# Kernel optimization log

Measured on AMD Instinct MI355X. Metric: run time of the kernel, lower is better.

The kernel has to match this reference:

```python
import jax, jax.numpy as jnp
import numpy as np

HEADS = 4
DIM_HEAD = 32


def setup_inputs() -> dict:
    key = jax.random.key(0)
    k1, k2, k3, k4 = jax.random.split(key, 4)
    b, dim, t = 8, 64, 16384
    inner = HEADS * DIM_HEAD  # 128
    x = jax.random.normal(k1, (b, dim, t), dtype=jnp.float32)
    # Conv1d(dim, inner*3, kernel=1, bias=False) -> weight (3*inner, dim)
    w_qkv = jax.random.normal(k2, (3 * inner, dim), dtype=jnp.float32) * (1.0 / np.sqrt(dim))
    # Conv1d(inner, dim, kernel=1) -> weight (dim, inner), bias (dim,)
    w_out = jax.random.normal(k3, (dim, inner), dtype=jnp.float32) * (1.0 / np.sqrt(inner))
    b_out = jax.random.normal(k4, (dim,), dtype=jnp.float32) * 0.01
    return {"x": x, "w_qkv": w_qkv, "w_out": w_out, "b_out": b_out}


def reference(x, w_qkv, w_out, b_out):
    b, c, t = x.shape
    h, dh = HEADS, DIM_HEAD
    # 1x1 conv == per-timestep matmul: (b, 3*inner, t)
    qkv = jnp.einsum('oc,bct->bot', w_qkv, x)
    q, k, v = jnp.split(qkv, 3, axis=1)
    q = q.reshape(b, h, dh, t)
    k = k.reshape(b, h, dh, t)
    v = v.reshape(b, h, dh, t)
    q = jax.nn.softmax(q, axis=-1)   # softmax over time
    k = jax.nn.softmax(k, axis=-2)   # softmax over head-dim d
    # einsum('bhdt,bhds->bhds', k, v): sums k over t, broadcast-scales v
    context = jnp.einsum('bhdt,bhds->bhds', k, v)
    # einsum('bhdt,bhds->bhdt', q, context): sums context over s, scales q
    out = jnp.einsum('bhdt,bhds->bhdt', q, context)
    out = out.reshape(b, h * dh, t)
    # to_out 1x1 conv with bias
    return jnp.einsum('oc,bct->bot', w_out, out) + b_out[None, :, None]
```

## Files before the change

### kernel.cpp

```cpp
#include <hip/hip_runtime.h>
#include <math.h>


typedef short short8 __attribute__((ext_vector_type(8)));
typedef short short4s __attribute__((ext_vector_type(4)));
typedef float f32x4 __attribute__((ext_vector_type(4)));

namespace {
constexpr int NB = 8;
constexpr int NC = 64;
constexpr int NT = 16384;
constexpr int NI = 128;
constexpr int TBLK = 128;
constexpr int NSTRIP = NT / TBLK;
constexpr int XSP = 72;
constexpr int PSP = 136;

constexpr int WS_KSUM = 0;
constexpr int WS_XSUM = WS_KSUM + NB * NI;
constexpr int WS_ZQ   = WS_XSUM + NB * NC;
constexpr int WS_NFLOAT = WS_ZQ + NB * NI;
}

__device__ __forceinline__ unsigned short f2bf(float f) {
  unsigned u = __float_as_uint(f);
  u += 0x7fffu + ((u >> 16) & 1u);
  return (unsigned short)(u >> 16);
}

template <bool XS>
__device__ __forceinline__ void stage_x(const float* __restrict__ xb, int t0,
                                        unsigned short* xs, float* xsum_g, int tid) {
  const int c = tid >> 2, tq = tid & 3;
  const float4* xr = (const float4*)(xb + (size_t)c * NT + t0);
  float s = 0.f;
#pragma unroll
  for (int i = 0; i < 8; ++i) {
    const int tv = tq + 4 * i;
    float4 v = xr[tv];
    if (XS) s += (v.x + v.y) + (v.z + v.w);
    const int t = tv * 4;
    xs[(t + 0) * XSP + c] = f2bf(v.x);
    xs[(t + 1) * XSP + c] = f2bf(v.y);
    xs[(t + 2) * XSP + c] = f2bf(v.z);
    xs[(t + 3) * XSP + c] = f2bf(v.w);
  }
  if (XS) {
    s += __shfl_xor(s, 1, 64);
    s += __shfl_xor(s, 2, 64);
    if (tq == 0) atomicAdd(xsum_g + c, s);
  }
}

__global__ __launch_bounds__(256) void la_stats(
    const float* __restrict__ x, const float* __restrict__ wqkv,
    float* __restrict__ ws)
{
  __shared__ __align__(16) unsigned short xs[TBLK * XSP];
  const int b = blockIdx.y, strip = blockIdx.x, tid = threadIdx.x;
  const int lane = tid & 63;
  const int h = __builtin_amdgcn_readfirstlane(tid >> 6);
  const int lm = lane & 15, quad = lane >> 4;
  const int t0 = strip * TBLK;
  const float* xb = x + (size_t)b * NC * NT;

  stage_x<true>(xb, t0, xs, ws + WS_XSUM + b * NC, tid);

  short8 aq[2][2], ak[2][2];
#pragma unroll
  for (int tile = 0; tile < 2; ++tile)
#pragma unroll
    for (int s = 0; s < 2; ++s) {
      const float* pq = wqkv + (size_t)(32 * h + tile * 16 + lm) * NC + s * 32 + quad * 8;
      const float* pk = wqkv + (size_t)(NI + 32 * h + tile * 16 + lm) * NC + s * 32 + quad * 8;
#pragma unroll
      for (int j = 0; j < 8; ++j) {
        aq[tile][s][j] = (short)f2bf(pq[j]);
        ak[tile][s][j] = (short)f2bf(pk[j]);
      }
    }

  float zq_acc[2][4] = {};
  float ks_acc[2][4] = {};
  __syncthreads();

  for (int tc = 0; tc < TBLK / 16; ++tc) {
    short8 bf[2];
#pragma unroll
    for (int s = 0; s < 2; ++s)
      bf[s] = *(const short8*)&xs[(tc * 16 + lm) * XSP + s * 32 + quad * 8];
    f32x4 cq[2] = {{0,0,0,0},{0,0,0,0}}, ck[2] = {{0,0,0,0},{0,0,0,0}};
#pragma unroll
    for (int tile = 0; tile < 2; ++tile)
#pragma unroll
      for (int s = 0; s < 2; ++s) {
        cq[tile] = __builtin_amdgcn_mfma_f32_16x16x32_bf16(aq[tile][s], bf[s], cq[tile], 0, 0, 0);
        ck[tile] = __builtin_amdgcn_mfma_f32_16x16x32_bf16(ak[tile][s], bf[s], ck[tile], 0, 0, 0);
      }
    float ke[2][4];
    float zt = 0.f;
#pragma unroll
    for (int tile = 0; tile < 2; ++tile)
#pragma unroll
      for (int r = 0; r < 4; ++r) {
        zq_acc[tile][r] += __expf(cq[tile][r]);
        float e = __expf(ck[tile][r]);
        ke[tile][r] = e;
        zt += e;
      }
    zt += __shfl_xor(zt, 16, 64);
    zt += __shfl_xor(zt, 32, 64);
    const float rz = __builtin_amdgcn_rcpf(zt);
#pragma unroll
    for (int tile = 0; tile < 2; ++tile)
#pragma unroll
      for (int r = 0; r < 4; ++r)
        ks_acc[tile][r] = fmaf(ke[tile][r], rz, ks_acc[tile][r]);
  }

#pragma unroll
  for (int tile = 0; tile < 2; ++tile)
#pragma unroll
    for (int r = 0; r < 4; ++r) {
      float a = zq_acc[tile][r], k = ks_acc[tile][r];
#pragma unroll
      for (int off = 1; off < 16; off <<= 1) {
        a += __shfl_xor(a, off, 64);
        k += __shfl_xor(k, off, 64);
      }
      zq_acc[tile][r] = a;
      ks_acc[tile][r] = k;
    }
  if (lm == 0) {
#pragma unroll
    for (int tile = 0; tile < 2; ++tile)
#pragma unroll
      for (int r = 0; r < 4; ++r) {
        const int c = 32 * h + tile * 16 + quad * 4 + r;
        atomicAdd(ws + WS_ZQ + b * NI + c, zq_acc[tile][r]);
        atomicAdd(ws + WS_KSUM + b * NI + c, ks_acc[tile][r]);
      }
  }
}

__global__ __launch_bounds__(256) void la_combine(
    const float* __restrict__ wqkv, const float* __restrict__ wout,
    float* __restrict__ ws, unsigned short* __restrict__ weff)
{
  const int b = blockIdx.x, tid = threadIdx.x;
  __shared__ float scale_s[NI];
  if (tid < NI) {
    const int c = tid;
    float vs = 0.f;
    for (int cc = 0; cc < NC; ++cc)
      vs = fmaf(wqkv[(size_t)(2 * NI + c) * NC + cc], ws[WS_XSUM + b * NC + cc], vs);
    scale_s[c] = ws[WS_KSUM + b * NI + c] * vs / ws[WS_ZQ + b * NI + c];
  }
  __syncthreads();
  const int o = tid >> 2, part = tid & 3;
  unsigned short* wb = weff + ((size_t)b * NC + o) * NI + part * 32;
  const float* wo = wout + (size_t)o * NI + part * 32;
#pragma unroll
  for (int i = 0; i < 32; ++i) wb[i] = f2bf(wo[i] * scale_s[part * 32 + i]);
}

__global__ __launch_bounds__(256) void la_out(
    const float* __restrict__ x, const float* __restrict__ wqkv,
    const float* __restrict__ bout, const unsigned short* __restrict__ weff,
    float* __restrict__ y)
{
  __shared__ __align__(16) unsigned short xs[TBLK * XSP];
  __shared__ __align__(16) unsigned short ps[TBLK * PSP];
  const int b = blockIdx.y, strip = blockIdx.x, tid = threadIdx.x;
  const int lane = tid & 63;
  const int w = __builtin_amdgcn_readfirstlane(tid >> 6);
  const int lm = lane & 15, quad = lane >> 4;
  const int t0 = strip * TBLK;
  const float* xb = x + (size_t)b * NC * NT;

  stage_x<false>(xb, t0, xs, nullptr, tid);

  short8 aq[2][2];
#pragma unroll
  for (int tile = 0; tile < 2; ++tile)
#pragma unroll
    for (int s = 0; s < 2; ++s) {
      const float* pq = wqkv + (size_t)(32 * w + tile * 16 + lm) * NC + s * 32 + quad * 8;
#pragma unroll
      for (int j = 0; j < 8; ++j) aq[tile][s][j] = (short)f2bf(pq[j]);
    }
  short8 aw[4];
#pragma unroll
  for (int s = 0; s < 4; ++s)
    aw[s] = *(const short8*)&weff[((size_t)b * NC + 16 * w + lm) * NI + s * 32 + quad * 8];
  float bias[4];
#pragma unroll
  for (int r = 0; r < 4; ++r) bias[r] = bout[16 * w + quad * 4 + r];

  __syncthreads();

  for (int tc = 0; tc < TBLK / 16; ++tc) {
    short8 bf[2];
#pragma unroll
    for (int s = 0; s < 2; ++s)
      bf[s] = *(const short8*)&xs[(tc * 16 + lm) * XSP + s * 32 + quad * 8];
    f32x4 cq[2] = {{0,0,0,0},{0,0,0,0}};
#pragma unroll
    for (int tile = 0; tile < 2; ++tile)
#pragma unroll
      for (int s = 0; s < 2; ++s)
        cq[tile] = __builtin_amdgcn_mfma_f32_16x16x32_bf16(aq[tile][s], bf[s], cq[tile], 0, 0, 0);
#pragma unroll
    for (int tile = 0; tile < 2; ++tile) {
      short4s pv;
#pragma unroll
      for (int r = 0; r < 4; ++r) pv[r] = (short)f2bf(__expf(cq[tile][r]));
      *(short4s*)&ps[(tc * 16 + lm) * PSP + 32 * w + tile * 16 + quad * 4] = pv;
    }
  }
  __syncthreads();

  for (int tc = 0; tc < TBLK / 16; ++tc) {
    short8 bp[4];
#pragma unroll
    for (int s = 0; s < 4; ++s)
      bp[s] = *(const short8*)&ps[(tc * 16 + lm) * PSP + s * 32 + quad * 8];
    f32x4 acc = {bias[0], bias[1], bias[2], bias[3]};
#pragma unroll
    for (int s = 0; s < 4; ++s)
      acc = __builtin_amdgcn_mfma_f32_16x16x32_bf16(aw[s], bp[s], acc, 0, 0, 0);
#pragma unroll
    for (int r = 0; r < 4; ++r)
      y[((size_t)b * NC + 16 * w + quad * 4 + r) * NT + t0 + tc * 16 + lm] = acc[r];
  }
}

extern "C" void kernel_launch(void* const* d_in, const int* in_sizes, int n_in,
                              void* d_out, int out_size, void* d_ws, size_t ws_size,
                              hipStream_t stream)
{
  const float* x    = (const float*)d_in[0];
  const float* wqkv = (const float*)d_in[1];
  const float* wout = (const float*)d_in[2];
  const float* bout = (const float*)d_in[3];
  float* y  = (float*)d_out;
  float* ws = (float*)d_ws;
  unsigned short* weff = (unsigned short*)(ws + WS_NFLOAT);

  hipMemsetAsync(ws, 0, (size_t)WS_NFLOAT * sizeof(float), stream);
  la_stats<<<dim3(NSTRIP, NB), 256, 0, stream>>>(x, wqkv, ws);
  la_combine<<<dim3(NB), 256, 0, stream>>>(wqkv, wout, ws, weff);
  la_out<<<dim3(NSTRIP, NB), 256, 0, stream>>>(x, wqkv, bout, weff, y);
}
```

Baseline: 133.3 us.

## Fold combine kernel into output pass and double time-chunk per block

Removes the separate la_combine launch. Each la_out block now recomputes the per-channel scale from workspace sums and builds the scaled bf16 output weights itself. Both passes move to 256-timestep chunks on a 1D grid, halving the block count. la_out also tiles the exp(q) staging into 32-step sub-tiles, which shrinks LDS but adds two barriers per sub-tile. The aim is to cut a launch and reduce atomics and per-block setup, at the cost of redundant scale computation in every block and lower parallelism (512 blocks).

```diff
diff --git a/kernel.cpp b/kernel.cpp
--- a/kernel.cpp
+++ b/kernel.cpp
@@ -11,15 +11,17 @@
 constexpr int NC = 64;
 constexpr int NT = 16384;
 constexpr int NI = 128;
-constexpr int TBLK = 128;
-constexpr int NSTRIP = NT / TBLK;
+constexpr int TBK = 256;
+constexpr int CPB = NT / TBK;
+constexpr int NBLK = NB * CPB;
 constexpr int XSP = 72;
-constexpr int PSP = 136;
-
-constexpr int WS_KSUM = 0;
+constexpr int PTP = 136;
+constexpr int PT  = 32;
+
+constexpr int WS_ZQ   = 0;
+constexpr int WS_KSUM = WS_ZQ + NB * NI;
 constexpr int WS_XSUM = WS_KSUM + NB * NI;
-constexpr int WS_ZQ   = WS_XSUM + NB * NC;
-constexpr int WS_NFLOAT = WS_ZQ + NB * NI;
+constexpr int WS_NFLOAT = WS_XSUM + NB * NC;
 }
 
 __device__ __forceinline__ unsigned short f2bf(float f) {
@@ -30,16 +32,16 @@
 
 template <bool XS>
 __device__ __forceinline__ void stage_x(const float* __restrict__ xb, int t0,
-                                        unsigned short* xs, float* xsum_g, int tid) {
+                                        unsigned short* xs, float* xsum_dst, int tid) {
   const int c = tid >> 2, tq = tid & 3;
   const float4* xr = (const float4*)(xb + (size_t)c * NT + t0);
   float s = 0.f;
-#pragma unroll
-  for (int i = 0; i < 8; ++i) {
+#pragma unroll 4
+  for (int i = 0; i < 16; ++i) {
     const int tv = tq + 4 * i;
     float4 v = xr[tv];
     if (XS) s += (v.x + v.y) + (v.z + v.w);
-    const int t = tv * 4;
+    const int t = 4 * tv;
     xs[(t + 0) * XSP + c] = f2bf(v.x);
     xs[(t + 1) * XSP + c] = f2bf(v.y);
     xs[(t + 2) * XSP + c] = f2bf(v.z);
@@ -48,43 +50,53 @@
   if (XS) {
     s += __shfl_xor(s, 1, 64);
     s += __shfl_xor(s, 2, 64);
-    if (tq == 0) atomicAdd(xsum_g + c, s);
-  }
+    if (tq == 0) atomicAdd(xsum_dst + c, s);
+  }
+}
+
+__device__ __forceinline__ void load_aq(const float* __restrict__ wqkv, int w,
+                                        int lm, int quad, short8 aq[2][2]) {
+#pragma unroll
+  for (int tile = 0; tile < 2; ++tile)
+#pragma unroll
+    for (int s = 0; s < 2; ++s) {
+      const float* pq = wqkv + (size_t)(32 * w + tile * 16 + lm) * NC + s * 32 + quad * 8;
+#pragma unroll
+      for (int j = 0; j < 8; ++j) aq[tile][s][j] = (short)f2bf(pq[j]);
+    }
 }
 
 __global__ __launch_bounds__(256) void la_stats(
     const float* __restrict__ x, const float* __restrict__ wqkv,
     float* __restrict__ ws)
 {
-  __shared__ __align__(16) unsigned short xs[TBLK * XSP];
-  const int b = blockIdx.y, strip = blockIdx.x, tid = threadIdx.x;
-  const int lane = tid & 63;
-  const int h = __builtin_amdgcn_readfirstlane(tid >> 6);
+  __shared__ __align__(16) unsigned short xs[TBK * XSP];
+
+  const int bid = blockIdx.x;
+  const int b = bid >> 6, chunk = bid & 63;
+  const int tid = threadIdx.x, lane = tid & 63;
+  const int w = __builtin_amdgcn_readfirstlane(tid >> 6);
   const int lm = lane & 15, quad = lane >> 4;
-  const int t0 = strip * TBLK;
   const float* xb = x + (size_t)b * NC * NT;
 
-  stage_x<true>(xb, t0, xs, ws + WS_XSUM + b * NC, tid);
+  stage_x<true>(xb, chunk * TBK, xs, ws + WS_XSUM + b * NC, tid);
 
   short8 aq[2][2], ak[2][2];
+  load_aq(wqkv, w, lm, quad, aq);
 #pragma unroll
   for (int tile = 0; tile < 2; ++tile)
 #pragma unroll
     for (int s = 0; s < 2; ++s) {
-      const float* pq = wqkv + (size_t)(32 * h + tile * 16 + lm) * NC + s * 32 + quad * 8;
-      const float* pk = wqkv + (size_t)(NI + 32 * h + tile * 16 + lm) * NC + s * 32 + quad * 8;
-#pragma unroll
-      for (int j = 0; j < 8; ++j) {
-        aq[tile][s][j] = (short)f2bf(pq[j]);
-        ak[tile][s][j] = (short)f2bf(pk[j]);
-      }
+      const float* pk = wqkv + (size_t)(NI + 32 * w + tile * 16 + lm) * NC + s * 32 + quad * 8;
+#pragma unroll
+      for (int j = 0; j < 8; ++j) ak[tile][s][j] = (short)f2bf(pk[j]);
     }
 
   float zq_acc[2][4] = {};
   float ks_acc[2][4] = {};
   __syncthreads();
 
-  for (int tc = 0; tc < TBLK / 16; ++tc) {
+  for (int tc = 0; tc < TBK / 16; ++tc) {
     short8 bf[2];
 #pragma unroll
     for (int s = 0; s < 2; ++s)
@@ -128,110 +140,98 @@
         a += __shfl_xor(a, off, 64);
         k += __shfl_xor(k, off, 64);
       }
-      zq_acc[tile][r] = a;
-      ks_acc[tile][r] = k;
-    }
-  if (lm == 0) {
-#pragma unroll
-    for (int tile = 0; tile < 2; ++tile)
-#pragma unroll
-      for (int r = 0; r < 4; ++r) {
-        const int c = 32 * h + tile * 16 + quad * 4 + r;
-        atomicAdd(ws + WS_ZQ + b * NI + c, zq_acc[tile][r]);
-        atomicAdd(ws + WS_KSUM + b * NI + c, ks_acc[tile][r]);
-      }
-  }
-}
-
-__global__ __launch_bounds__(256) void la_combine(
-    const float* __restrict__ wqkv, const float* __restrict__ wout,
-    float* __restrict__ ws, unsigned short* __restrict__ weff)
-{
-  const int b = blockIdx.x, tid = threadIdx.x;
-  __shared__ float scale_s[NI];
-  if (tid < NI) {
-    const int c = tid;
-    float vs = 0.f;
-    for (int cc = 0; cc < NC; ++cc)
-      vs = fmaf(wqkv[(size_t)(2 * NI + c) * NC + cc], ws[WS_XSUM + b * NC + cc], vs);
-    scale_s[c] = ws[WS_KSUM + b * NI + c] * vs / ws[WS_ZQ + b * NI + c];
-  }
-  __syncthreads();
-  const int o = tid >> 2, part = tid & 3;
-  unsigned short* wb = weff + ((size_t)b * NC + o) * NI + part * 32;
-  const float* wo = wout + (size_t)o * NI + part * 32;
-#pragma unroll
-  for (int i = 0; i < 32; ++i) wb[i] = f2bf(wo[i] * scale_s[part * 32 + i]);
+      if (lm == 0) {
+        const int c = 32 * w + tile * 16 + quad * 4 + r;
+        atomicAdd(ws + WS_ZQ + b * NI + c, a);
+        atomicAdd(ws + WS_KSUM + b * NI + c, k);
+      }
+    }
 }
 
 __global__ __launch_bounds__(256) void la_out(
     const float* __restrict__ x, const float* __restrict__ wqkv,
-    const float* __restrict__ bout, const unsigned short* __restrict__ weff,
-    float* __restrict__ y)
+    const float* __restrict__ wout, const float* __restrict__ bout,
+    const float* __restrict__ ws, float* __restrict__ y)
 {
-  __shared__ __align__(16) unsigned short xs[TBLK * XSP];
-  __shared__ __align__(16) unsigned short ps[TBLK * PSP];
-  const int b = blockIdx.y, strip = blockIdx.x, tid = threadIdx.x;
-  const int lane = tid & 63;
+  __shared__ __align__(16) unsigned short xs[TBK * XSP];
+  __shared__ __align__(16) unsigned short pt[PT * PTP];
+  __shared__ float scale_s[NI];
+  __shared__ float xsum_s[NC];
+
+  const int bid = blockIdx.x;
+  const int b = bid >> 6, chunk = bid & 63;
+  const int tid = threadIdx.x, lane = tid & 63;
   const int w = __builtin_amdgcn_readfirstlane(tid >> 6);
   const int lm = lane & 15, quad = lane >> 4;
-  const int t0 = strip * TBLK;
+  const int t0 = chunk * TBK;
   const float* xb = x + (size_t)b * NC * NT;
 
   stage_x<false>(xb, t0, xs, nullptr, tid);
 
+  if (tid < NC) xsum_s[tid] = ws[WS_XSUM + b * NC + tid];
+  __syncthreads();
+  if (tid < NI) {
+    float vs = 0.f;
+    const float* wv = wqkv + (size_t)(2 * NI + tid) * NC;
+#pragma unroll 8
+    for (int cc = 0; cc < NC; ++cc) vs = fmaf(wv[cc], xsum_s[cc], vs);
+    scale_s[tid] = ws[WS_KSUM + b * NI + tid] * vs / ws[WS_ZQ + b * NI + tid];
+  }
+  __syncthreads();
+
   short8 aq[2][2];
-#pragma unroll
-  for (int tile = 0; tile < 2; ++tile)
-#pragma unroll
-    for (int s = 0; s < 2; ++s) {
-      const float* pq = wqkv + (size_t)(32 * w + tile * 16 + lm) * NC + s * 32 + quad * 8;
-#pragma unroll
-      for (int j = 0; j < 8; ++j) aq[tile][s][j] = (short)f2bf(pq[j]);
-    }
+  load_aq(wqkv, w, lm, quad, aq);
   short8 aw[4];
-#pragma unroll
-  for (int s = 0; s < 4; ++s)
-    aw[s] = *(const short8*)&weff[((size_t)b * NC + 16 * w + lm) * NI + s * 32 + quad * 8];
+  {
+    const int o = 16 * w + lm;
+#pragma unroll
+    for (int s = 0; s < 4; ++s) {
+      const float* wo = wout + (size_t)o * NI + s * 32 + quad * 8;
+#pragma unroll
+      for (int j = 0; j < 8; ++j)
+        aw[s][j] = (short)f2bf(wo[j] * scale_s[s * 32 + quad * 8 + j]);
+    }
+  }
   float bias[4];
 #pragma unroll
   for (int r = 0; r < 4; ++r) bias[r] = bout[16 * w + quad * 4 + r];
 
-  __syncthreads();
-
-  for (int tc = 0; tc < TBLK / 16; ++tc) {
-    short8 bf[2];
-#pragma unroll
-    for (int s = 0; s < 2; ++s)
-      bf[s] = *(const short8*)&xs[(tc * 16 + lm) * XSP + s * 32 + quad * 8];
-    f32x4 cq[2] = {{0,0,0,0},{0,0,0,0}};
-#pragma unroll
-    for (int tile = 0; tile < 2; ++tile)
+  for (int sub = 0; sub < TBK / PT; ++sub) {
+    for (int tc = 0; tc < PT / 16; ++tc) {
+      const int tl = sub * PT + tc * 16;
+      short8 bf[2];
 #pragma unroll
       for (int s = 0; s < 2; ++s)
-        cq[tile] = __builtin_amdgcn_mfma_f32_16x16x32_bf16(aq[tile][s], bf[s], cq[tile], 0, 0, 0);
-#pragma unroll
-    for (int tile = 0; tile < 2; ++tile) {
-      short4s pv;
-#pragma unroll
-      for (int r = 0; r < 4; ++r) pv[r] = (short)f2bf(__expf(cq[tile][r]));
-      *(short4s*)&ps[(tc * 16 + lm) * PSP + 32 * w + tile * 16 + quad * 4] = pv;
-    }
-  }
-  __syncthreads();
-
-  for (int tc = 0; tc < TBLK / 16; ++tc) {
-    short8 bp[4];
-#pragma unroll
-    for (int s = 0; s < 4; ++s)
-      bp[s] = *(const short8*)&ps[(tc * 16 + lm) * PSP + s * 32 + quad * 8];
-    f32x4 acc = {bias[0], bias[1], bias[2], bias[3]};
-#pragma unroll
-    for (int s = 0; s < 4; ++s)
-      acc = __builtin_amdgcn_mfma_f32_16x16x32_bf16(aw[s], bp[s], acc, 0, 0, 0);
-#pragma unroll
-    for (int r = 0; r < 4; ++r)
-      y[((size_t)b * NC + 16 * w + quad * 4 + r) * NT + t0 + tc * 16 + lm] = acc[r];
+        bf[s] = *(const short8*)&xs[(tl + lm) * XSP + s * 32 + quad * 8];
+      f32x4 cq[2] = {{0,0,0,0},{0,0,0,0}};
+#pragma unroll
+      for (int tile = 0; tile < 2; ++tile)
+#pragma unroll
+        for (int s = 0; s < 2; ++s)
+          cq[tile] = __builtin_amdgcn_mfma_f32_16x16x32_bf16(aq[tile][s], bf[s], cq[tile], 0, 0, 0);
+#pragma unroll
+      for (int tile = 0; tile < 2; ++tile) {
+        short4s pv;
+#pragma unroll
+        for (int r = 0; r < 4; ++r) pv[r] = (short)f2bf(__expf(cq[tile][r]));
+        *(short4s*)&pt[(tc * 16 + lm) * PTP + 32 * w + tile * 16 + quad * 4] = pv;
+      }
+    }
+    __syncthreads();
+    for (int tc = 0; tc < PT / 16; ++tc) {
+      short8 bp[4];
+#pragma unroll
+      for (int s = 0; s < 4; ++s)
+        bp[s] = *(const short8*)&pt[(tc * 16 + lm) * PTP + s * 32 + quad * 8];
+      f32x4 acc = {bias[0], bias[1], bias[2], bias[3]};
+#pragma unroll
+      for (int s = 0; s < 4; ++s)
+        acc = __builtin_amdgcn_mfma_f32_16x16x32_bf16(aw[s], bp[s], acc, 0, 0, 0);
+#pragma unroll
+      for (int r = 0; r < 4; ++r)
+        y[((size_t)b * NC + 16 * w + quad * 4 + r) * NT + t0 + sub * PT + tc * 16 + lm] = acc[r];
+    }
+    __syncthreads();
   }
 }
 
@@ -245,10 +245,10 @@
   const float* bout = (const float*)d_in[3];
   float* y  = (float*)d_out;
   float* ws = (float*)d_ws;
-  unsigned short* weff = (unsigned short*)(ws + WS_NFLOAT);
+
+  if (ws_size < (size_t)WS_NFLOAT * sizeof(float)) return;
 
   hipMemsetAsync(ws, 0, (size_t)WS_NFLOAT * sizeof(float), stream);
-  la_stats<<<dim3(NSTRIP, NB), 256, 0, stream>>>(x, wqkv, ws);
-  la_combine<<<dim3(NB), 256, 0, stream>>>(wqkv, wout, ws, weff);
-  la_out<<<dim3(NSTRIP, NB), 256, 0, stream>>>(x, wqkv, bout, weff, y);
-}
+  la_stats<<<dim3(NBLK), 256, 0, stream>>>(x, wqkv, ws);
+  la_out<<<dim3(NBLK), 256, 0, stream>>>(x, wqkv, wout, bout, ws, y);
+}
```

Result: faster. 118.8 us (-10.9%).
